# Optimization experiments

Measured on AMD Instinct MI355X. Metric: run time of the kernel, lower is better.

The kernel has to match this reference:

```python
import jax, jax.numpy as jnp
import numpy as np

N_NODES = 40000
N_EDGES = 640000
IN_DIM, H_DIM, OUT_DIM = 128, 128, 64


def setup_inputs() -> dict:
    key = jax.random.key(0)
    ks = jax.random.split(key, 16)
    x = jax.random.normal(ks[0], (N_NODES, IN_DIM), dtype=jnp.float32)
    edge_index = jax.random.randint(ks[1], (2, N_EDGES), 0, N_NODES, dtype=jnp.int64)
    dims = [(IN_DIM, H_DIM), (H_DIM, H_DIM), (H_DIM, OUT_DIM)]
    inp = {"x": x, "edge_index": edge_index}
    for l, (di, do) in enumerate(dims):
        s = 1.0 / np.sqrt(di)
        inp[f"Wr{l}"] = jax.random.uniform(ks[2 + 3 * l], (di, do), jnp.float32, -s, s)  # lin_rel weight
        inp[f"br{l}"] = jax.random.uniform(ks[3 + 3 * l], (do,), jnp.float32, -s, s)     # lin_rel bias
        inp[f"Ws{l}"] = jax.random.uniform(ks[4 + 3 * l], (di, do), jnp.float32, -s, s)  # lin_root weight (no bias)
    return inp


def _graph_conv(x, src, dst, Wr, br, Ws):
    # PyG GraphConv (aggr='add'): out = lin_rel(sum_{j in N(i)} x_j) + lin_root(x_i)
    agg = jax.ops.segment_sum(x[src], dst, num_segments=N_NODES)  # [N, d_in]
    return agg @ Wr + br + x @ Ws


def reference(x, edge_index, Wr0, br0, Ws0, Wr1, br1, Ws1, Wr2, br2, Ws2):
    src, dst = edge_index[0], edge_index[1]
    h = x
    for Wr, br, Ws in ((Wr0, br0, Ws0), (Wr1, br1, Ws1), (Wr2, br2, Ws2)):
        h = _graph_conv(h, src, dst, Wr, br, Ws)
        h = jax.nn.relu(h)
        # dropout p=0 / eval mode -> identity
    return jax.nn.log_softmax(h, axis=1)
```

## Files before the change

kernel.cpp:

```cpp
#include <hip/hip_runtime.h>
#include <hip/hip_bf16.h>


#define N_NODES 40000
#define N_EDGES 640000
#define PAD_NODES 40064
#define DEG_CAP   40960
#define ROW_CAP   64
#define QPLANE    (40064 * 32)

typedef float v4f __attribute__((ext_vector_type(4)));
typedef float v2f __attribute__((ext_vector_type(2)));
typedef short short8 __attribute__((ext_vector_type(8)));

__device__ inline unsigned short f2b(float f) {
    unsigned u = __float_as_uint(f);
    return (unsigned short)((u + 0x7fffu + ((u >> 16) & 1u)) >> 16);
}

__global__ __launch_bounds__(256) void prep_kernel(const float* __restrict__ Wr0, const float* __restrict__ Ws0,
                                                   const float* __restrict__ Wr1, const float* __restrict__ Ws1,
                                                   const float* __restrict__ Wr2, const float* __restrict__ Ws2,
                                                   unsigned short* __restrict__ Wt0,
                                                   unsigned short* __restrict__ Wt1,
                                                   unsigned short* __restrict__ Wt2,
                                                   int* __restrict__ deg) {
    int tid = blockIdx.x * 256 + threadIdx.x;
    if (tid < DEG_CAP / 4) {
        ((int4*)deg)[tid] = make_int4(0, 0, 0, 0);
    } else {
        int t = tid - DEG_CAP / 4;
        if (t < 32768) {
            int n = t >> 7, k = t & 127;
            const float* W = (n < 128) ? Wr0 : Ws0;
            Wt0[t] = f2b(W[k * 128 + (n & 127)]);
        } else if (t < 65536) {
            int u = t - 32768;
            int n = u >> 7, k = u & 127;
            const float* W = (n < 128) ? Wr1 : Ws1;
            Wt1[u] = f2b(W[k * 128 + (n & 127)]);
        } else if (t < 81920) {
            int u = t - 65536;
            int n = u >> 7, k = u & 127;
            const float* W = (n < 64) ? Wr2 : Ws2;
            Wt2[u] = f2b(W[k * 64 + (n & 63)]);
        }
    }
}

__global__ __launch_bounds__(256) void place_kernel(const int* __restrict__ src,
                                                    const int* __restrict__ dst,
                                                    int* __restrict__ deg,
                                                    unsigned short* __restrict__ esrc) {
    int e = blockIdx.x * 256 + threadIdx.x;
    if (e < N_EDGES) {
        int d = dst[e];
        int r = atomicAdd(&deg[d], 1);
        if (r < ROW_CAP) esrc[(size_t)d * ROW_CAP + r] = (unsigned short)src[e];
    }
}

template <int DO, bool F32>
__global__ __launch_bounds__(256, 3) void mm_kernel(const void* __restrict__ Ain,
                                                    const unsigned short* __restrict__ Wt,
                                                    unsigned short* __restrict__ T,
                                                    unsigned short* __restrict__ S) {
    __shared__ unsigned short As[128 * 64];
    __shared__ unsigned short Bs[128 * 64];

    const int tid = threadIdx.x;
    const int m0  = blockIdx.x * 128;
    const int n0  = blockIdx.y * 128;

    const int wave = tid >> 6;
    const int lane = tid & 63;
    const int wr   = (wave >> 1) * 64;
    const int wc   = (wave & 1) * 64;
    const int qm   = lane & 15;
    const int k8   = (lane >> 4) * 8;

    v4f acc[4][4];
#pragma unroll
    for (int i = 0; i < 4; i++)
#pragma unroll
        for (int j = 0; j < 4; j++) acc[i][j] = (v4f)(0.0f);

#pragma unroll
    for (int half = 0; half < 2; half++) {
        if (F32) {
            const float4* Xg = (const float4*)Ain;
#pragma unroll
            for (int i = 0; i < 8; i++) {
                int idx = i * 256 + tid;
                int row = idx >> 4, c4 = idx & 15;
                int gr = m0 + row;
                if (gr > N_NODES - 1) gr = N_NODES - 1;
                float4 v = Xg[(size_t)gr * 32 + half * 16 + c4];
                uint2 p;
                p.x = (unsigned)f2b(v.x) | ((unsigned)f2b(v.y) << 16);
                p.y = (unsigned)f2b(v.z) | ((unsigned)f2b(v.w) << 16);
                ((uint2*)As)[idx] = p;
            }
        } else {
            const unsigned short* Ab = (const unsigned short*)Ain;
#pragma unroll
            for (int i = 0; i < 4; i++) {
                int idx = i * 256 + tid;
                int row = idx >> 3, c8 = idx & 7;
                ((uint4*)As)[idx] =
                    *(const uint4*)(Ab + (size_t)(m0 + row) * 128 + half * 64 + c8 * 8);
            }
        }
        {
#pragma unroll
            for (int i = 0; i < 4; i++) {
                int idx = i * 256 + tid;
                int row = idx >> 3, c8 = idx & 7;
                ((uint4*)Bs)[idx] =
                    *(const uint4*)(Wt + (size_t)(n0 + row) * 128 + half * 64 + c8 * 8);
            }
        }
        __syncthreads();

#pragma unroll
        for (int ks = 0; ks < 2; ks++) {
            short8 af[4], bf[4];
#pragma unroll
            for (int i = 0; i < 4; i++) {
                af[i] = *(const short8*)(const void*)(As + (wr + i * 16 + qm) * 64 + ks * 32 + k8);
                bf[i] = *(const short8*)(const void*)(Bs + (wc + i * 16 + qm) * 64 + ks * 32 + k8);
            }
#pragma unroll
            for (int mi = 0; mi < 4; mi++)
#pragma unroll
                for (int ni = 0; ni < 4; ni++)
                    acc[mi][ni] = __builtin_amdgcn_mfma_f32_16x16x32_bf16(af[mi], bf[ni], acc[mi][ni], 0, 0, 0);
        }
        __syncthreads();
    }

#pragma unroll
    for (int mi = 0; mi < 4; mi++) {
        const int nodeBase = m0 + wr + mi * 16 + ((lane >> 4) << 2);
#pragma unroll
        for (int r = 0; r < 4; r++) {
            const int node = nodeBase + r;
            if (node <= N_NODES) {
                const bool real = (node < N_NODES);
#pragma unroll
                for (int ni = 0; ni < 4; ni++) {
                    const int c = wc + ni * 16 + qm;
                    const unsigned short hv = real ? f2b(acc[mi][ni][r]) : (unsigned short)0;
                    if (DO == 128) {
                        if (n0) S[(size_t)node * 128 + c] = hv;
                        else    T[(size_t)(c >> 5) * QPLANE + (size_t)node * 32 + (c & 31)] = hv;
                    } else {
                        if (c < 64) T[(size_t)node * 64 + c] = hv;
                        else        S[(size_t)node * 64 + (c - 64)] = hv;
                    }
                }
            }
        }
    }
}

__device__ inline void addp(v2f* a, uint4 q) {
    v2f t0 = { __uint_as_float(q.x << 16), __uint_as_float(q.x & 0xffff0000u) };
    v2f t1 = { __uint_as_float(q.y << 16), __uint_as_float(q.y & 0xffff0000u) };
    v2f t2 = { __uint_as_float(q.z << 16), __uint_as_float(q.z & 0xffff0000u) };
    v2f t3 = { __uint_as_float(q.w << 16), __uint_as_float(q.w & 0xffff0000u) };
    a[0] += t0; a[1] += t1; a[2] += t2; a[3] += t3;
}

__global__ __launch_bounds__(256) void aggregate_q_kernel(const unsigned short* __restrict__ T,
                                                          const unsigned short* __restrict__ S,
                                                          const float* __restrict__ br,
                                                          const int* __restrict__ deg,
                                                          const unsigned short* __restrict__ esrc,
                                                          unsigned short* __restrict__ Hout) {
    const int bid = blockIdx.x;
    const int q   = (bid & 7) >> 1;
    const int s   = (bid >> 3) * 2 + (bid & 1);
    if (s >= N_NODES / 64) return;
    const int lane4 = threadIdx.x & 3;
    const int n     = s * 64 + (threadIdx.x >> 2);

    int cnt = deg[n];
    if (cnt > ROW_CAP) cnt = ROW_CAP;
    const unsigned short* erow = esrc + (size_t)n * ROW_CAP;
    const uint4* T4 = (const uint4*)(T + (size_t)q * QPLANE);

    const uint4  sv = ((const uint4*)S)[(size_t)n * 16 + q * 4 + lane4];
    const float4 b0 = ((const float4*)br)[q * 8 + lane4 * 2];
    const float4 b1 = ((const float4*)br)[q * 8 + lane4 * 2 + 1];

    v2f acc[4];
    acc[0] = (v2f)(0.0f); acc[1] = (v2f)(0.0f);
    acc[2] = (v2f)(0.0f); acc[3] = (v2f)(0.0f);

    for (int o = 0; o < cnt; o += 8) {
        uint4 iv = *(const uint4*)(erow + o);
        unsigned j0 = iv.x & 0xffffu, j1 = iv.x >> 16;
        unsigned j2 = iv.y & 0xffffu, j3 = iv.y >> 16;
        unsigned j4 = iv.z & 0xffffu, j5 = iv.z >> 16;
        unsigned j6 = iv.w & 0xffffu, j7 = iv.w >> 16;
        j0 = (o + 0 < cnt) ? j0 : N_NODES;
        j1 = (o + 1 < cnt) ? j1 : N_NODES;
        j2 = (o + 2 < cnt) ? j2 : N_NODES;
        j3 = (o + 3 < cnt) ? j3 : N_NODES;
        j4 = (o + 4 < cnt) ? j4 : N_NODES;
        j5 = (o + 5 < cnt) ? j5 : N_NODES;
        j6 = (o + 6 < cnt) ? j6 : N_NODES;
        j7 = (o + 7 < cnt) ? j7 : N_NODES;
        uint4 q0 = T4[(size_t)j0 * 4 + lane4];
        uint4 q1 = T4[(size_t)j1 * 4 + lane4];
        uint4 q2 = T4[(size_t)j2 * 4 + lane4];
        uint4 q3 = T4[(size_t)j3 * 4 + lane4];
        uint4 q4 = T4[(size_t)j4 * 4 + lane4];
        uint4 q5 = T4[(size_t)j5 * 4 + lane4];
        uint4 q6 = T4[(size_t)j6 * 4 + lane4];
        uint4 q7 = T4[(size_t)j7 * 4 + lane4];
        addp(acc, q0); addp(acc, q1); addp(acc, q2); addp(acc, q3);
        addp(acc, q4); addp(acc, q5); addp(acc, q6); addp(acc, q7);
    }
    addp(acc, sv);

    float v[8];
    v[0] = fmaxf(acc[0].x + b0.x, 0.f); v[1] = fmaxf(acc[0].y + b0.y, 0.f);
    v[2] = fmaxf(acc[1].x + b0.z, 0.f); v[3] = fmaxf(acc[1].y + b0.w, 0.f);
    v[4] = fmaxf(acc[2].x + b1.x, 0.f); v[5] = fmaxf(acc[2].y + b1.y, 0.f);
    v[6] = fmaxf(acc[3].x + b1.z, 0.f); v[7] = fmaxf(acc[3].y + b1.w, 0.f);

    uint4 o;
    o.x = (unsigned)f2b(v[0]) | ((unsigned)f2b(v[1]) << 16);
    o.y = (unsigned)f2b(v[2]) | ((unsigned)f2b(v[3]) << 16);
    o.z = (unsigned)f2b(v[4]) | ((unsigned)f2b(v[5]) << 16);
    o.w = (unsigned)f2b(v[6]) | ((unsigned)f2b(v[7]) << 16);
    ((uint4*)Hout)[(size_t)n * 16 + q * 4 + lane4] = o;
}

__global__ __launch_bounds__(256) void aggregate_last_kernel(const unsigned short* __restrict__ T,
                                                             const unsigned short* __restrict__ S,
                                                             const float* __restrict__ br,
                                                             const int* __restrict__ deg,
                                                             const unsigned short* __restrict__ esrc,
                                                             float* __restrict__ Fout) {
    constexpr int TPN = 8;
    const int lane = threadIdx.x % TPN;
    const int n    = blockIdx.x * 32 + threadIdx.x / TPN;

    int cnt = deg[n];
    if (cnt > ROW_CAP) cnt = ROW_CAP;
    const unsigned short* erow = esrc + (size_t)n * ROW_CAP;
    const uint4* T4 = (const uint4*)T;

    const uint4  sv = ((const uint4*)S)[(size_t)n * TPN + lane];
    const float4 b0 = ((const float4*)br)[lane * 2];
    const float4 b1 = ((const float4*)br)[lane * 2 + 1];

    v2f acc[4];
    acc[0] = (v2f)(0.0f); acc[1] = (v2f)(0.0f);
    acc[2] = (v2f)(0.0f); acc[3] = (v2f)(0.0f);

    for (int o = 0; o < cnt; o += 8) {
        uint4 iv = *(const uint4*)(erow + o);
        unsigned j0 = iv.x & 0xffffu, j1 = iv.x >> 16;
        unsigned j2 = iv.y & 0xffffu, j3 = iv.y >> 16;
        unsigned j4 = iv.z & 0xffffu, j5 = iv.z >> 16;
        unsigned j6 = iv.w & 0xffffu, j7 = iv.w >> 16;
        j0 = (o + 0 < cnt) ? j0 : N_NODES;
        j1 = (o + 1 < cnt) ? j1 : N_NODES;
        j2 = (o + 2 < cnt) ? j2 : N_NODES;
        j3 = (o + 3 < cnt) ? j3 : N_NODES;
        j4 = (o + 4 < cnt) ? j4 : N_NODES;
        j5 = (o + 5 < cnt) ? j5 : N_NODES;
        j6 = (o + 6 < cnt) ? j6 : N_NODES;
        j7 = (o + 7 < cnt) ? j7 : N_NODES;
        uint4 q0 = T4[(size_t)j0 * TPN + lane];
        uint4 q1 = T4[(size_t)j1 * TPN + lane];
        uint4 q2 = T4[(size_t)j2 * TPN + lane];
        uint4 q3 = T4[(size_t)j3 * TPN + lane];
        uint4 q4 = T4[(size_t)j4 * TPN + lane];
        uint4 q5 = T4[(size_t)j5 * TPN + lane];
        uint4 q6 = T4[(size_t)j6 * TPN + lane];
        uint4 q7 = T4[(size_t)j7 * TPN + lane];
        addp(acc, q0); addp(acc, q1); addp(acc, q2); addp(acc, q3);
        addp(acc, q4); addp(acc, q5); addp(acc, q6); addp(acc, q7);
    }
    addp(acc, sv);

    float v[8];
    v[0] = fmaxf(acc[0].x + b0.x, 0.f); v[1] = fmaxf(acc[0].y + b0.y, 0.f);
    v[2] = fmaxf(acc[1].x + b0.z, 0.f); v[3] = fmaxf(acc[1].y + b0.w, 0.f);
    v[4] = fmaxf(acc[2].x + b1.x, 0.f); v[5] = fmaxf(acc[2].y + b1.y, 0.f);
    v[6] = fmaxf(acc[3].x + b1.z, 0.f); v[7] = fmaxf(acc[3].y + b1.w, 0.f);

    float m = v[0];
#pragma unroll
    for (int i = 1; i < 8; i++) m = fmaxf(m, v[i]);
#pragma unroll
    for (int off = 4; off; off >>= 1) m = fmaxf(m, __shfl_xor(m, off, 64));
    float es = 0.f;
#pragma unroll
    for (int i = 0; i < 8; i++) es += expf(v[i] - m);
#pragma unroll
    for (int off = 4; off; off >>= 1) es += __shfl_xor(es, off, 64);
    float lse = m + logf(es);
    float4 o0 = make_float4(v[0] - lse, v[1] - lse, v[2] - lse, v[3] - lse);
    float4 o1 = make_float4(v[4] - lse, v[5] - lse, v[6] - lse, v[7] - lse);
    ((float4*)Fout)[(size_t)n * 16 + lane * 2]     = o0;
    ((float4*)Fout)[(size_t)n * 16 + lane * 2 + 1] = o1;
}


extern "C" void kernel_launch(void* const* d_in, const int* in_sizes, int n_in,
                              void* d_out, int out_size, void* d_ws, size_t ws_size,
                              hipStream_t stream) {
    const float* x    = (const float*)d_in[0];
    const int*   eidx = (const int*)d_in[1];
    const float* Wr0  = (const float*)d_in[2];
    const float* br0  = (const float*)d_in[3];
    const float* Ws0  = (const float*)d_in[4];
    const float* Wr1  = (const float*)d_in[5];
    const float* br1  = (const float*)d_in[6];
    const float* Ws1  = (const float*)d_in[7];
    const float* Wr2  = (const float*)d_in[8];
    const float* br2  = (const float*)d_in[9];
    const float* Ws2  = (const float*)d_in[10];
    float* out = (float*)d_out;

    const int* src = eidx;
    const int* dst = eidx + N_EDGES;

    auto align = [](size_t v) { return (v + 255) & ~(size_t)255; };
    char* w = (char*)d_ws;
    int* deg  = (int*)w;             w += align(sizeof(int) * DEG_CAP);
    unsigned short* esrc = (unsigned short*)w;
    w += align(sizeof(unsigned short) * (size_t)N_NODES * ROW_CAP);
    unsigned short* H1b = (unsigned short*)w;  w += align(2ull * PAD_NODES * 128);
    unsigned short* H2b = (unsigned short*)w;  w += align(2ull * PAD_NODES * 128);
    unsigned short* Wt0 = (unsigned short*)w;  w += align(2ull * 256 * 128);
    unsigned short* Wt1 = (unsigned short*)w;  w += align(2ull * 256 * 128);
    unsigned short* Wt2 = (unsigned short*)w;  w += align(2ull * 128 * 128);
    unsigned short* T   = (unsigned short*)w;  w += align(2ull * PAD_NODES * 128);
    unsigned short* Sb  = (unsigned short*)w;  w += align(2ull * PAD_NODES * 128);
    (void)ws_size; (void)n_in; (void)in_sizes; (void)out_size;

    prep_kernel<<<(DEG_CAP / 4 + 81920 + 255) / 256, 256, 0, stream>>>(
        Wr0, Ws0, Wr1, Ws1, Wr2, Ws2, Wt0, Wt1, Wt2, deg);

    place_kernel<<<(N_EDGES + 255) / 256, 256, 0, stream>>>(src, dst, deg, esrc);

    mm_kernel<128, true><<<dim3(PAD_NODES / 128, 2), 256, 0, stream>>>(x, Wt0, T, Sb);
    aggregate_q_kernel<<<2504, 256, 0, stream>>>(T, Sb, br0, deg, esrc, H1b);

    mm_kernel<128, false><<<dim3(PAD_NODES / 128, 2), 256, 0, stream>>>(H1b, Wt1, T, Sb);
    aggregate_q_kernel<<<2504, 256, 0, stream>>>(T, Sb, br1, deg, esrc, H2b);

    mm_kernel<64, false><<<dim3(PAD_NODES / 128, 1), 256, 0, stream>>>(H2b, Wt2, T, Sb);
    aggregate_last_kernel<<<N_NODES / 32, 256, 0, stream>>>(T, Sb, br2, deg, esrc, out);
}
```

Measured before the change: 216.8 us.

## Use nontemporal loads/stores and split aggregation into per-quarter launches

```diff
diff --git a/kernel.cpp b/kernel.cpp
--- a/kernel.cpp
+++ b/kernel.cpp
@@ -12,6 +12,10 @@
 typedef float v4f __attribute__((ext_vector_type(4)));
 typedef float v2f __attribute__((ext_vector_type(2)));
 typedef short short8 __attribute__((ext_vector_type(8)));
+typedef unsigned u32x4 __attribute__((ext_vector_type(4)));
+
+#define NTL(p)    __builtin_nontemporal_load(p)
+#define NTS(v, p) __builtin_nontemporal_store(v, p)
 
 __device__ inline unsigned short f2b(float f) {
     unsigned u = __float_as_uint(f);
@@ -54,9 +58,10 @@
                                                     unsigned short* __restrict__ esrc) {
     int e = blockIdx.x * 256 + threadIdx.x;
     if (e < N_EDGES) {
-        int d = dst[e];
+        int d = NTL(dst + e);
+        int s = NTL(src + e);
         int r = atomicAdd(&deg[d], 1);
-        if (r < ROW_CAP) esrc[(size_t)d * ROW_CAP + r] = (unsigned short)src[e];
+        if (r < ROW_CAP) NTS((unsigned short)s, &esrc[(size_t)d * ROW_CAP + r]);
     }
 }
 
@@ -152,11 +157,11 @@
                     const int c = wc + ni * 16 + qm;
                     const unsigned short hv = real ? f2b(acc[mi][ni][r]) : (unsigned short)0;
                     if (DO == 128) {
-                        if (n0) S[(size_t)node * 128 + c] = hv;
-                        else    T[(size_t)(c >> 5) * QPLANE + (size_t)node * 32 + (c & 31)] = hv;
+                        if (n0) NTS(hv, &S[(size_t)node * 128 + c]);
+                        else    NTS(hv, &T[(size_t)(c >> 5) * QPLANE + (size_t)node * 32 + (c & 31)]);
                     } else {
-                        if (c < 64) T[(size_t)node * 64 + c] = hv;
-                        else        S[(size_t)node * 64 + (c - 64)] = hv;
+                        if (c < 64) NTS(hv, &T[(size_t)node * 64 + c]);
+                        else        NTS(hv, &S[(size_t)node * 64 + (c - 64)]);
                     }
                 }
             }
@@ -164,7 +169,7 @@
     }
 }
 
-__device__ inline void addp(v2f* a, uint4 q) {
+__device__ inline void addp(v2f* a, u32x4 q) {
     v2f t0 = { __uint_as_float(q.x << 16), __uint_as_float(q.x & 0xffff0000u) };
     v2f t1 = { __uint_as_float(q.y << 16), __uint_as_float(q.y & 0xffff0000u) };
     v2f t2 = { __uint_as_float(q.z << 16), __uint_as_float(q.z & 0xffff0000u) };
@@ -172,25 +177,23 @@
     a[0] += t0; a[1] += t1; a[2] += t2; a[3] += t3;
 }
 
-__global__ __launch_bounds__(256) void aggregate_q_kernel(const unsigned short* __restrict__ T,
+__global__ __launch_bounds__(128) void aggregate_q_kernel(const unsigned short* __restrict__ T,
                                                           const unsigned short* __restrict__ S,
                                                           const float* __restrict__ br,
                                                           const int* __restrict__ deg,
                                                           const unsigned short* __restrict__ esrc,
-                                                          unsigned short* __restrict__ Hout) {
-    const int bid = blockIdx.x;
-    const int q   = (bid & 7) >> 1;
-    const int s   = (bid >> 3) * 2 + (bid & 1);
-    if (s >= N_NODES / 64) return;
+                                                          unsigned short* __restrict__ Hout,
+                                                          int q) {
     const int lane4 = threadIdx.x & 3;
-    const int n     = s * 64 + (threadIdx.x >> 2);
+    const int n     = blockIdx.x * 32 + (threadIdx.x >> 2);
+    if (n >= N_NODES) return;
 
     int cnt = deg[n];
     if (cnt > ROW_CAP) cnt = ROW_CAP;
     const unsigned short* erow = esrc + (size_t)n * ROW_CAP;
-    const uint4* T4 = (const uint4*)(T + (size_t)q * QPLANE);
-
-    const uint4  sv = ((const uint4*)S)[(size_t)n * 16 + q * 4 + lane4];
+    const u32x4* T4 = (const u32x4*)(T + (size_t)q * QPLANE);
+
+    const u32x4  sv = NTL((const u32x4*)S + (size_t)n * 16 + q * 4 + lane4);
     const float4 b0 = ((const float4*)br)[q * 8 + lane4 * 2];
     const float4 b1 = ((const float4*)br)[q * 8 + lane4 * 2 + 1];
 
@@ -199,7 +202,7 @@
     acc[2] = (v2f)(0.0f); acc[3] = (v2f)(0.0f);
 
     for (int o = 0; o < cnt; o += 8) {
-        uint4 iv = *(const uint4*)(erow + o);
+        u32x4 iv = NTL((const u32x4*)(const void*)(erow + o));
         unsigned j0 = iv.x & 0xffffu, j1 = iv.x >> 16;
         unsigned j2 = iv.y & 0xffffu, j3 = iv.y >> 16;
         unsigned j4 = iv.z & 0xffffu, j5 = iv.z >> 16;
@@ -212,14 +215,14 @@
         j5 = (o + 5 < cnt) ? j5 : N_NODES;
         j6 = (o + 6 < cnt) ? j6 : N_NODES;
         j7 = (o + 7 < cnt) ? j7 : N_NODES;
-        uint4 q0 = T4[(size_t)j0 * 4 + lane4];
-        uint4 q1 = T4[(size_t)j1 * 4 + lane4];
-        uint4 q2 = T4[(size_t)j2 * 4 + lane4];
-        uint4 q3 = T4[(size_t)j3 * 4 + lane4];
-        uint4 q4 = T4[(size_t)j4 * 4 + lane4];
-        uint4 q5 = T4[(size_t)j5 * 4 + lane4];
-        uint4 q6 = T4[(size_t)j6 * 4 + lane4];
-        uint4 q7 = T4[(size_t)j7 * 4 + lane4];
+        u32x4 q0 = T4[(size_t)j0 * 4 + lane4];
+        u32x4 q1 = T4[(size_t)j1 * 4 + lane4];
+        u32x4 q2 = T4[(size_t)j2 * 4 + lane4];
+        u32x4 q3 = T4[(size_t)j3 * 4 + lane4];
+        u32x4 q4 = T4[(size_t)j4 * 4 + lane4];
+        u32x4 q5 = T4[(size_t)j5 * 4 + lane4];
+        u32x4 q6 = T4[(size_t)j6 * 4 + lane4];
+        u32x4 q7 = T4[(size_t)j7 * 4 + lane4];
         addp(acc, q0); addp(acc, q1); addp(acc, q2); addp(acc, q3);
         addp(acc, q4); addp(acc, q5); addp(acc, q6); addp(acc, q7);
     }
@@ -231,12 +234,12 @@
     v[4] = fmaxf(acc[2].x + b1.x, 0.f); v[5] = fmaxf(acc[2].y + b1.y, 0.f);
     v[6] = fmaxf(acc[3].x + b1.z, 0.f); v[7] = fmaxf(acc[3].y + b1.w, 0.f);
 
-    uint4 o;
+    u32x4 o;
     o.x = (unsigned)f2b(v[0]) | ((unsigned)f2b(v[1]) << 16);
     o.y = (unsigned)f2b(v[2]) | ((unsigned)f2b(v[3]) << 16);
     o.z = (unsigned)f2b(v[4]) | ((unsigned)f2b(v[5]) << 16);
     o.w = (unsigned)f2b(v[6]) | ((unsigned)f2b(v[7]) << 16);
-    ((uint4*)Hout)[(size_t)n * 16 + q * 4 + lane4] = o;
+    NTS(o, (u32x4*)Hout + (size_t)n * 16 + q * 4 + lane4);
 }
 
 __global__ __launch_bounds__(256) void aggregate_last_kernel(const unsigned short* __restrict__ T,
@@ -252,9 +255,9 @@
     int cnt = deg[n];
     if (cnt > ROW_CAP) cnt = ROW_CAP;
     const unsigned short* erow = esrc + (size_t)n * ROW_CAP;
-    const uint4* T4 = (const uint4*)T;
-
-    const uint4  sv = ((const uint4*)S)[(size_t)n * TPN + lane];
+    const u32x4* T4 = (const u32x4*)T;
+
+    const u32x4  sv = NTL((const u32x4*)S + (size_t)n * TPN + lane);
     const float4 b0 = ((const float4*)br)[lane * 2];
     const float4 b1 = ((const float4*)br)[lane * 2 + 1];
 
@@ -263,7 +266,7 @@
     acc[2] = (v2f)(0.0f); acc[3] = (v2f)(0.0f);
 
     for (int o = 0; o < cnt; o += 8) {
-        uint4 iv = *(const uint4*)(erow + o);
+        u32x4 iv = NTL((const u32x4*)(const void*)(erow + o));
         unsigned j0 = iv.x & 0xffffu, j1 = iv.x >> 16;
         unsigned j2 = iv.y & 0xffffu, j3 = iv.y >> 16;
         unsigned j4 = iv.z & 0xffffu, j5 = iv.z >> 16;
@@ -276,14 +279,14 @@
         j5 = (o + 5 < cnt) ? j5 : N_NODES;
         j6 = (o + 6 < cnt) ? j6 : N_NODES;
         j7 = (o + 7 < cnt) ? j7 : N_NODES;
-        uint4 q0 = T4[(size_t)j0 * TPN + lane];
-        uint4 q1 = T4[(size_t)j1 * TPN + lane];
-        uint4 q2 = T4[(size_t)j2 * TPN + lane];
-        uint4 q3 = T4[(size_t)j3 * TPN + lane];
-        uint4 q4 = T4[(size_t)j4 * TPN + lane];
-        uint4 q5 = T4[(size_t)j5 * TPN + lane];
-        uint4 q6 = T4[(size_t)j6 * TPN + lane];
-        uint4 q7 = T4[(size_t)j7 * TPN + lane];
+        u32x4 q0 = T4[(size_t)j0 * TPN + lane];
+        u32x4 q1 = T4[(size_t)j1 * TPN + lane];
+        u32x4 q2 = T4[(size_t)j2 * TPN + lane];
+        u32x4 q3 = T4[(size_t)j3 * TPN + lane];
+        u32x4 q4 = T4[(size_t)j4 * TPN + lane];
+        u32x4 q5 = T4[(size_t)j5 * TPN + lane];
+        u32x4 q6 = T4[(size_t)j6 * TPN + lane];
+        u32x4 q7 = T4[(size_t)j7 * TPN + lane];
         addp(acc, q0); addp(acc, q1); addp(acc, q2); addp(acc, q3);
         addp(acc, q4); addp(acc, q5); addp(acc, q6); addp(acc, q7);
     }
@@ -306,10 +309,10 @@
 #pragma unroll
     for (int off = 4; off; off >>= 1) es += __shfl_xor(es, off, 64);
     float lse = m + logf(es);
-    float4 o0 = make_float4(v[0] - lse, v[1] - lse, v[2] - lse, v[3] - lse);
-    float4 o1 = make_float4(v[4] - lse, v[5] - lse, v[6] - lse, v[7] - lse);
-    ((float4*)Fout)[(size_t)n * 16 + lane * 2]     = o0;
-    ((float4*)Fout)[(size_t)n * 16 + lane * 2 + 1] = o1;
+    v4f o0 = { v[0] - lse, v[1] - lse, v[2] - lse, v[3] - lse };
+    v4f o1 = { v[4] - lse, v[5] - lse, v[6] - lse, v[7] - lse };
+    NTS(o0, (v4f*)Fout + (size_t)n * 16 + lane * 2);
+    NTS(o1, (v4f*)Fout + (size_t)n * 16 + lane * 2 + 1);
 }
 
 
@@ -352,10 +355,12 @@
     place_kernel<<<(N_EDGES + 255) / 256, 256, 0, stream>>>(src, dst, deg, esrc);
 
     mm_kernel<128, true><<<dim3(PAD_NODES / 128, 2), 256, 0, stream>>>(x, Wt0, T, Sb);
-    aggregate_q_kernel<<<2504, 256, 0, stream>>>(T, Sb, br0, deg, esrc, H1b);
+    for (int q = 0; q < 4; q++)
+        aggregate_q_kernel<<<1252, 128, 0, stream>>>(T, Sb, br0, deg, esrc, H1b, q);
 
     mm_kernel<128, false><<<dim3(PAD_NODES / 128, 2), 256, 0, stream>>>(H1b, Wt1, T, Sb);
-    aggregate_q_kernel<<<2504, 256, 0, stream>>>(T, Sb, br1, deg, esrc, H2b);
+    for (int q = 0; q < 4; q++)
+        aggregate_q_kernel<<<1252, 128, 0, stream>>>(T, Sb, br1, deg, esrc, H2b, q);
 
     mm_kernel<64, false><<<dim3(PAD_NODES / 128, 1), 256, 0, stream>>>(H2b, Wt2, T, Sb);
     aggregate_last_kernel<<<N_NODES / 32, 256, 0, stream>>>(T, Sb, br2, deg, esrc, out);
```

After: 272.7 us. 1.26x slower.
